# Kernel optimization log

Measured on AMD Instinct MI355X. Metric: run time of the kernel, lower is better.

Reference implementation:

```python
import jax, jax.numpy as jnp
import numpy as np

MIN_DURATION = 0.0
MAX_DURATION = 75.0
MAX_LEN = 80  # hard-coded output length from regulate_length's slice/pad to 80
LN_EPS = 1e-6


def _conv1d_same(x, w, b):
    # x: [B, T, Cin], w: [K, Cin, Cout] -> [B, T, Cout]
    y = jax.lax.conv_general_dilated(
        x, w, window_strides=(1,), padding='SAME',
        dimension_numbers=('NWC', 'WIO', 'NWC'))
    return y + b


def _layernorm(x, gamma, beta):
    mu = jnp.mean(x, axis=-1, keepdims=True)
    var = jnp.mean(jnp.square(x - mu), axis=-1, keepdims=True)
    return (x - mu) * jax.lax.rsqrt(var + LN_EPS) * gamma + beta


def setup_inputs() -> dict:
    key = jax.random.key(0)
    ks = jax.random.split(key, 5)
    B, T, D, F, K = 2048, 128, 256, 256, 3
    scale = 0.05
    return {
        'encoder_output': jax.random.normal(ks[0], (B, T, D), jnp.float32),
        'conv1_w': jax.random.normal(ks[1], (K, D, F), jnp.float32) * scale,
        'conv1_b': jnp.zeros((F,), jnp.float32),
        'conv2_w': jax.random.normal(ks[2], (K, F, F), jnp.float32) * scale,
        'conv2_b': jnp.zeros((F,), jnp.float32),
        'ln_gamma': jnp.ones((F,), jnp.float32),
        'ln_beta': jnp.zeros((F,), jnp.float32),
        'dense_w': jax.random.normal(ks[3], (F, 1), jnp.float32) * scale,
        'dense_b': jnp.full((1,), 2.0, jnp.float32),  # bias so rounded durations are nontrivial
    }


def reference(encoder_output, conv1_w, conv1_b, conv2_w, conv2_b,
              ln_gamma, ln_beta, dense_w, dense_b):
    # --- variance predictor (dropout = identity at inference) ---
    x = jax.nn.relu(_conv1d_same(encoder_output, conv1_w, conv1_b))
    x = _layernorm(x, ln_gamma, ln_beta)
    x = jax.nn.relu(_conv1d_same(x, conv2_w, conv2_b))
    x = _layernorm(x, ln_gamma, ln_beta)
    predicted_durations = x @ dense_w + dense_b  # [B, T, 1]

    # --- regulate_length, fully vectorized over batch ---
    dur = jnp.round(jnp.clip(predicted_durations, MIN_DURATION, MAX_DURATION))
    dur = dur[..., 0].astype(jnp.int32)                 # [B, T]
    cum = jnp.cumsum(dur, axis=1)                       # [B, T]
    pos = jnp.arange(MAX_LEN, dtype=jnp.int32)          # [80]
    # source index for each output frame: searchsorted(cum, pos, side='right')
    idx = jnp.sum(pos[None, :, None] >= cum[:, None, :], axis=-1)  # [B, 80]
    valid = pos[None, :] < cum[:, -1:]                  # [B, 80]
    T = encoder_output.shape[1]
    gathered = jnp.take_along_axis(
        encoder_output, jnp.clip(idx, 0, T - 1)[..., None], axis=1)  # [B, 80, D]
    regulated = jnp.where(valid[..., None], gathered, 0.0)
    return regulated
```

## Files before the change

### kernel.cpp

```cpp
#include <hip/hip_runtime.h>
#include <hip/hip_bf16.h>
#include <math.h>

#define TT 128
#define CC 256
#define MAXLEN 80
#define KSTEPS 24
#define SLOTS 130
#define NCH16 32

typedef __attribute__((ext_vector_type(8))) _Float16 half8v;
typedef __attribute__((ext_vector_type(4))) float f32x4;

#define MSCALE 4096.0f
#define MINV   (1.0f/4096.0f)

__device__ __forceinline__ int chunk(int slot, int c16) {
    return slot * NCH16 + (c16 ^ (slot & 7));
}

__global__ void va_prep(const float* __restrict__ w1, const float* __restrict__ w2,
                        half8v* __restrict__ wsB)
{
    const int idx = blockIdx.x * 256 + threadIdx.x;
    const int lane = idx & 63;
    int q = idx >> 6;
    const int nfg = q & 15;   q >>= 4;
    const int plane = q & 1;  q >>= 1;
    const int kk2 = q & 7;    q >>= 3;
    const int tap = q % 3;
    const int cv  = q / 3;
    const float* w = cv ? w2 : w1;
    const int co  = nfg * 16 + (lane & 15);
    const int ci0 = kk2 * 32 + (lane >> 4) * 8;
    half8v out;
    #pragma unroll
    for (int j = 0; j < 8; ++j) {
        const float x = w[tap * (CC * CC) + (ci0 + j) * CC + co];
        const _Float16 h = (_Float16)x;
        if (plane == 0) out[j] = h;
        else            out[j] = (_Float16)((x - (float)h) * MSCALE);
    }
    wsB[idx] = out;
}

__global__ __launch_bounds__(512, 2)
void va_mfma(const float* __restrict__ enc,
             const float* __restrict__ b1g, const float* __restrict__ b2g,
             const float* __restrict__ gg,  const float* __restrict__ bbg,
             const float* __restrict__ dwg, const float* __restrict__ dbg,
             const half8v* __restrict__ wsB,
             float* __restrict__ outg)
{
    __shared__ half8v P[2][SLOTS * NCH16];
    __shared__ float sumS[8][TT];
    __shared__ float muS[TT];
    __shared__ float rsS[TT];
    __shared__ int   durS[TT];
    __shared__ int   cumS[TT];
    __shared__ int   wtotS[2];

    const int b    = blockIdx.x;
    const int tid  = threadIdx.x;
    const int wid  = tid >> 6;
    const int lane = tid & 63;
    const int l15  = lane & 15;
    const int lg   = lane >> 4;

    const f32x4* encB4 = reinterpret_cast<const f32x4*>(enc) + (size_t)b * (TT * 64);

    for (int m = tid; m < SLOTS * NCH16; m += 512) {
        const int slot = m >> 5;
        const int c16  = m & 31;
        half8v h8, m8;
        if (slot >= 1 && slot <= TT) {
            const f32x4* src = encB4 + (slot - 1) * 64 + c16 * 2;
            const f32x4 v0 = src[0], v1 = src[1];
            #pragma unroll
            for (int j = 0; j < 8; ++j) {
                const float x = (j < 4) ? v0[j] : v1[j - 4];
                const _Float16 h = (_Float16)x;
                h8[j] = h;
                m8[j] = (_Float16)((x - (float)h) * MSCALE);
            }
        } else {
            #pragma unroll
            for (int j = 0; j < 8; ++j) { h8[j] = (_Float16)0.f; m8[j] = (_Float16)0.f; }
        }
        const int ci = chunk(slot, c16);
        P[0][ci] = h8;
        P[1][ci] = m8;
    }
    __syncthreads();

    f32x4 accH[8][2];
    f32x4 accM[8][2];

    float gv[2], bvv[2];
    #pragma unroll
    for (int nf = 0; nf < 2; ++nf) {
        gv[nf]  = gg[wid * 32 + nf * 16 + l15];
        bvv[nf] = bbg[wid * 32 + nf * 16 + l15];
    }

    auto convpass = [&](int cv, const float* __restrict__ biasp, bool first) {
        #pragma unroll
        for (int nf = 0; nf < 2; ++nf) {
            const float bz = biasp[wid * 32 + nf * 16 + l15];
            const f32x4 b4 = {bz, bz, bz, bz};
            const f32x4 z4 = {0.f, 0.f, 0.f, 0.f};
            #pragma unroll
            for (int mf = 0; mf < 8; ++mf) { accH[mf][nf] = b4; accM[mf][nf] = z4; }
        }

        half8v B0[4], B1[4];
        auto loadB = [&](half8v (&Bp)[4], int ks) {
            const int tap = ks >> 3, kk2 = ks & 7;
            #pragma unroll
            for (int p = 0; p < 2; ++p) {
                const int frag = (((cv * 3 + tap) * 8 + kk2) * 2 + p);
                #pragma unroll
                for (int nf = 0; nf < 2; ++nf)
                    Bp[p * 2 + nf] = wsB[(size_t)(frag * 16 + (wid * 2 + nf)) * 64 + lane];
            }
        };
        auto doK = [&](const half8v (&Bp)[4], int ks) {
            const int tap = ks >> 3, kk2 = ks & 7;
            #pragma unroll
            for (int mf = 0; mf < 8; ++mf) {
                const int slot = mf * 16 + l15 + tap;
                const int c16  = kk2 * 4 + lg;
                const int ci = chunk(slot, c16);
                const half8v Ah = P[0][ci];
                const half8v Am = P[1][ci];
                #pragma unroll
                for (int nf = 0; nf < 2; ++nf) {
                    accH[mf][nf] = __builtin_amdgcn_mfma_f32_16x16x32_f16(Ah, Bp[0 * 2 + nf], accH[mf][nf], 0, 0, 0);
                    accM[mf][nf] = __builtin_amdgcn_mfma_f32_16x16x32_f16(Ah, Bp[1 * 2 + nf], accM[mf][nf], 0, 0, 0);
                    accM[mf][nf] = __builtin_amdgcn_mfma_f32_16x16x32_f16(Am, Bp[0 * 2 + nf], accM[mf][nf], 0, 0, 0);
                }
            }
        };

        loadB(B0, 0);
        #pragma unroll 1
        for (int ks = 0; ks < KSTEPS; ks += 2) {
            loadB(B1, ks + 1);
            doK(B0, ks);
            if (ks + 2 < KSTEPS) loadB(B0, ks + 2);
            doK(B1, ks + 1);
        }

        #pragma unroll
        for (int mf = 0; mf < 8; ++mf)
            #pragma unroll
            for (int nf = 0; nf < 2; ++nf) {
                f32x4 v;
                #pragma unroll
                for (int e = 0; e < 4; ++e)
                    v[e] = fmaxf(fmaf(accM[mf][nf][e], MINV, accH[mf][nf][e]), 0.f);
                accH[mf][nf] = v;
            }

        #pragma unroll
        for (int mf = 0; mf < 8; ++mf)
            #pragma unroll
            for (int r = 0; r < 4; ++r) {
                float s = accH[mf][0][r] + accH[mf][1][r];
                s += __shfl_xor(s, 1, 64); s += __shfl_xor(s, 2, 64);
                s += __shfl_xor(s, 4, 64); s += __shfl_xor(s, 8, 64);
                if (l15 == 0) sumS[wid][mf * 16 + lg * 4 + r] = s;
            }
        __syncthreads();
        if (tid < TT) {
            float t = 0.f;
            #pragma unroll
            for (int w = 0; w < 8; ++w) t += sumS[w][tid];
            muS[tid] = t * (1.f / 256.f);
        }
        __syncthreads();
        #pragma unroll
        for (int mf = 0; mf < 8; ++mf)
            #pragma unroll
            for (int r = 0; r < 4; ++r) {
                const float mu = muS[mf * 16 + lg * 4 + r];
                float q = 0.f;
                #pragma unroll
                for (int nf = 0; nf < 2; ++nf) {
                    const float d = accH[mf][nf][r] - mu;
                    q = fmaf(d, d, q);
                }
                q += __shfl_xor(q, 1, 64); q += __shfl_xor(q, 2, 64);
                q += __shfl_xor(q, 4, 64); q += __shfl_xor(q, 8, 64);
                if (l15 == 0) sumS[wid][mf * 16 + lg * 4 + r] = q;
            }
        __syncthreads();
        if (tid < TT) {
            float t = 0.f;
            #pragma unroll
            for (int w = 0; w < 8; ++w) t += sumS[w][tid];
            rsS[tid] = 1.0f / sqrtf(t * (1.f / 256.f) + 1e-6f);
        }
        __syncthreads();
        _Float16* Ph = (_Float16*)&P[0][0];
        _Float16* Pm = (_Float16*)&P[1][0];
        #pragma unroll
        for (int mf = 0; mf < 8; ++mf)
            #pragma unroll
            for (int r = 0; r < 4; ++r) {
                const int row = mf * 16 + lg * 4 + r;
                const float mu = muS[row];
                const float rs = rsS[row];
                #pragma unroll
                for (int nf = 0; nf < 2; ++nf) {
                    const float v = (accH[mf][nf][r] - mu) * rs * gv[nf] + bvv[nf];
                    if (first) {
                        const int col = wid * 32 + nf * 16 + l15;
                        const int slot = row + 1;
                        const int off = chunk(slot, col >> 3) * 8 + (col & 7);
                        const _Float16 h = (_Float16)v;
                        Ph[off] = h;
                        Pm[off] = (_Float16)((v - (float)h) * MSCALE);
                    } else {
                        accH[mf][nf][r] = v;
                    }
                }
            }
    };

    convpass(0, b1g, true);
    __syncthreads();
    convpass(1, b2g, false);

    {
        float dv[2];
        #pragma unroll
        for (int nf = 0; nf < 2; ++nf) dv[nf] = dwg[wid * 32 + nf * 16 + l15];
        #pragma unroll
        for (int mf = 0; mf < 8; ++mf)
            #pragma unroll
            for (int r = 0; r < 4; ++r) {
                float p = accH[mf][0][r] * dv[0] + accH[mf][1][r] * dv[1];
                p += __shfl_xor(p, 1, 64); p += __shfl_xor(p, 2, 64);
                p += __shfl_xor(p, 4, 64); p += __shfl_xor(p, 8, 64);
                if (l15 == 0) sumS[wid][mf * 16 + lg * 4 + r] = p;
            }
        __syncthreads();
        if (tid < TT) {
            float t = 0.f;
            #pragma unroll
            for (int w = 0; w < 8; ++w) t += sumS[w][tid];
            const float pd  = t + dbg[0];
            const float dcl = fminf(fmaxf(pd, 0.0f), 75.0f);
            durS[tid] = (int)rintf(dcl);
        }
        __syncthreads();
    }

    int sv = 0;
    if (tid < TT) {
        sv = durS[tid];
        #pragma unroll
        for (int o = 1; o < 64; o <<= 1) {
            const int u = __shfl_up(sv, o, 64);
            if (lane >= o) sv += u;
        }
        if (lane == 63) wtotS[tid >> 6] = sv;
    }
    __syncthreads();
    if (tid < TT) {
        if (tid >= 64) sv += wtotS[0];
        cumS[tid] = sv;
    }
    __syncthreads();

    const int total = cumS[TT - 1];
    f32x4* outB4 = reinterpret_cast<f32x4*>(outg) + (size_t)b * (MAXLEN * 64);
    for (int pp = 0; pp < 10; ++pp) {
        const int p = wid * 10 + pp;
        int lo = 0, hi = TT;
        while (lo < hi) {
            const int mid = (lo + hi) >> 1;
            if (cumS[mid] <= p) lo = mid + 1; else hi = mid;
        }
        f32x4 v = {0.f, 0.f, 0.f, 0.f};
        if (p < total) {
            const int src = (lo < TT) ? lo : (TT - 1);
            v = encB4[src * 64 + lane];
        }
        outB4[p * 64 + lane] = v;
    }
}

extern "C" void kernel_launch(void* const* d_in, const int* in_sizes, int n_in,
                              void* d_out, int out_size, void* d_ws, size_t ws_size,
                              hipStream_t stream) {
    const float* enc = (const float*)d_in[0];
    const float* w1  = (const float*)d_in[1];
    const float* b1  = (const float*)d_in[2];
    const float* w2  = (const float*)d_in[3];
    const float* b2  = (const float*)d_in[4];
    const float* gam = (const float*)d_in[5];
    const float* bet = (const float*)d_in[6];
    const float* dw  = (const float*)d_in[7];
    const float* db  = (const float*)d_in[8];
    float* out = (float*)d_out;
    half8v* wsB = (half8v*)d_ws;

    const int B = in_sizes[0] / (TT * CC);
    hipLaunchKernelGGL(va_prep, dim3(384), dim3(256), 0, stream, w1, w2, wsB);
    hipLaunchKernelGGL(va_mfma, dim3(B), dim3(512), 0, stream,
                       enc, b1, b2, gam, bet, dw, db, wsB, out);
}
```

Measured before the change: 771.8 us.

## Retile conv MFMA warps to 2x4 grid and fuse layernorm statistics pass

Changes the per-warp tile from all 128 rows by 32 columns to 64 rows by 64 columns (2 row groups by 4 column groups). Each LDS A-fragment read now feeds four N-fragments instead of two, which roughly halves LDS traffic per MFMA. Global weight loads per warp double. Layernorm mean and variance are now computed in one pass as sum and sum of squares, which removes two barriers but risks cancellation error in E[x^2]-mu^2. The fp16 hi/lo split now uses a packed cvt_pkrtz conversion, whose round-toward-zero rounding differs from the old round-to-nearest cast.

```diff
diff --git a/kernel.cpp b/kernel.cpp
--- a/kernel.cpp
+++ b/kernel.cpp
@@ -10,13 +10,20 @@
 #define NCH16 32
 
 typedef __attribute__((ext_vector_type(8))) _Float16 half8v;
+typedef __attribute__((ext_vector_type(2))) _Float16 half2v;
 typedef __attribute__((ext_vector_type(4))) float f32x4;
 
 #define MSCALE 4096.0f
 #define MINV   (1.0f/4096.0f)
 
-__device__ __forceinline__ int chunk(int slot, int c16) {
+__device__ __forceinline__ int chunkidx(int slot, int c16) {
     return slot * NCH16 + (c16 ^ (slot & 7));
+}
+
+__device__ __forceinline__ void split2(float x0, float x1, half2v& h, half2v& m) {
+    h = __builtin_bit_cast(half2v, __builtin_amdgcn_cvt_pkrtz(x0, x1));
+    m.x = (_Float16)fmaf((float)h.x, -MSCALE, x0 * MSCALE);
+    m.y = (_Float16)fmaf((float)h.y, -MSCALE, x1 * MSCALE);
 }
 
 __global__ void va_prep(const float* __restrict__ w1, const float* __restrict__ w2,
@@ -53,7 +60,8 @@
              float* __restrict__ outg)
 {
     __shared__ half8v P[2][SLOTS * NCH16];
-    __shared__ float sumS[8][TT];
+    __shared__ float sumS[4][TT];
+    __shared__ float sumQ[4][TT];
     __shared__ float muS[TT];
     __shared__ float rsS[TT];
     __shared__ int   durS[TT];
@@ -66,78 +74,78 @@
     const int lane = tid & 63;
     const int l15  = lane & 15;
     const int lg   = lane >> 4;
+    const int MGr  = (wid >> 2) * 64;
+    const int NG   = wid & 3;
+    const int NGc  = NG * 64;
 
     const f32x4* encB4 = reinterpret_cast<const f32x4*>(enc) + (size_t)b * (TT * 64);
 
-    for (int m = tid; m < SLOTS * NCH16; m += 512) {
-        const int slot = m >> 5;
-        const int c16  = m & 31;
+    for (int m2 = tid; m2 < SLOTS * NCH16; m2 += 512) {
+        const int slot = m2 >> 5;
+        const int c16  = m2 & 31;
         half8v h8, m8;
         if (slot >= 1 && slot <= TT) {
             const f32x4* src = encB4 + (slot - 1) * 64 + c16 * 2;
             const f32x4 v0 = src[0], v1 = src[1];
-            #pragma unroll
-            for (int j = 0; j < 8; ++j) {
-                const float x = (j < 4) ? v0[j] : v1[j - 4];
-                const _Float16 h = (_Float16)x;
-                h8[j] = h;
-                m8[j] = (_Float16)((x - (float)h) * MSCALE);
-            }
+            half2v hp, mp;
+            split2(v0.x, v0.y, hp, mp); h8[0]=hp.x; h8[1]=hp.y; m8[0]=mp.x; m8[1]=mp.y;
+            split2(v0.z, v0.w, hp, mp); h8[2]=hp.x; h8[3]=hp.y; m8[2]=mp.x; m8[3]=mp.y;
+            split2(v1.x, v1.y, hp, mp); h8[4]=hp.x; h8[5]=hp.y; m8[4]=mp.x; m8[5]=mp.y;
+            split2(v1.z, v1.w, hp, mp); h8[6]=hp.x; h8[7]=hp.y; m8[6]=mp.x; m8[7]=mp.y;
         } else {
             #pragma unroll
             for (int j = 0; j < 8; ++j) { h8[j] = (_Float16)0.f; m8[j] = (_Float16)0.f; }
         }
-        const int ci = chunk(slot, c16);
+        const int ci = chunkidx(slot, c16);
         P[0][ci] = h8;
         P[1][ci] = m8;
     }
     __syncthreads();
 
-    f32x4 accH[8][2];
-    f32x4 accM[8][2];
-
-    float gv[2], bvv[2];
+    f32x4 accH[4][4];
+    f32x4 accM[4][4];
+
+    float gv[4], bvv[4];
     #pragma unroll
-    for (int nf = 0; nf < 2; ++nf) {
-        gv[nf]  = gg[wid * 32 + nf * 16 + l15];
-        bvv[nf] = bbg[wid * 32 + nf * 16 + l15];
+    for (int nf = 0; nf < 4; ++nf) {
+        gv[nf]  = gg[NGc + nf * 16 + l15];
+        bvv[nf] = bbg[NGc + nf * 16 + l15];
     }
 
     auto convpass = [&](int cv, const float* __restrict__ biasp, bool first) {
         #pragma unroll
-        for (int nf = 0; nf < 2; ++nf) {
-            const float bz = biasp[wid * 32 + nf * 16 + l15];
+        for (int nf = 0; nf < 4; ++nf) {
+            const float bz = biasp[NGc + nf * 16 + l15];
             const f32x4 b4 = {bz, bz, bz, bz};
             const f32x4 z4 = {0.f, 0.f, 0.f, 0.f};
             #pragma unroll
-            for (int mf = 0; mf < 8; ++mf) { accH[mf][nf] = b4; accM[mf][nf] = z4; }
-        }
-
-        half8v B0[4], B1[4];
-        auto loadB = [&](half8v (&Bp)[4], int ks) {
+            for (int mf = 0; mf < 4; ++mf) { accH[mf][nf] = b4; accM[mf][nf] = z4; }
+        }
+
+        half8v B0[8], B1[8];
+        auto loadB = [&](half8v (&Bp)[8], int ks) {
             const int tap = ks >> 3, kk2 = ks & 7;
-            #pragma unroll
-            for (int p = 0; p < 2; ++p) {
-                const int frag = (((cv * 3 + tap) * 8 + kk2) * 2 + p);
-                #pragma unroll
-                for (int nf = 0; nf < 2; ++nf)
-                    Bp[p * 2 + nf] = wsB[(size_t)(frag * 16 + (wid * 2 + nf)) * 64 + lane];
-            }
+            const int fb = ((cv * 3 + tap) * 8 + kk2) * 2;
+            #pragma unroll
+            for (int p = 0; p < 2; ++p)
+                #pragma unroll
+                for (int nf = 0; nf < 4; ++nf)
+                    Bp[p * 4 + nf] = wsB[(size_t)((fb + p) * 16 + (NG * 4 + nf)) * 64 + lane];
         };
-        auto doK = [&](const half8v (&Bp)[4], int ks) {
+        auto doK = [&](const half8v (&Bp)[8], int ks) {
             const int tap = ks >> 3, kk2 = ks & 7;
             #pragma unroll
-            for (int mf = 0; mf < 8; ++mf) {
-                const int slot = mf * 16 + l15 + tap;
+            for (int mf = 0; mf < 4; ++mf) {
+                const int slot = MGr + mf * 16 + l15 + tap;
                 const int c16  = kk2 * 4 + lg;
-                const int ci = chunk(slot, c16);
+                const int ci = chunkidx(slot, c16);
                 const half8v Ah = P[0][ci];
                 const half8v Am = P[1][ci];
                 #pragma unroll
-                for (int nf = 0; nf < 2; ++nf) {
-                    accH[mf][nf] = __builtin_amdgcn_mfma_f32_16x16x32_f16(Ah, Bp[0 * 2 + nf], accH[mf][nf], 0, 0, 0);
-                    accM[mf][nf] = __builtin_amdgcn_mfma_f32_16x16x32_f16(Ah, Bp[1 * 2 + nf], accM[mf][nf], 0, 0, 0);
-                    accM[mf][nf] = __builtin_amdgcn_mfma_f32_16x16x32_f16(Am, Bp[0 * 2 + nf], accM[mf][nf], 0, 0, 0);
+                for (int nf = 0; nf < 4; ++nf) {
+                    accH[mf][nf] = __builtin_amdgcn_mfma_f32_16x16x32_f16(Ah, Bp[nf],     accH[mf][nf], 0, 0, 0);
+                    accM[mf][nf] = __builtin_amdgcn_mfma_f32_16x16x32_f16(Ah, Bp[4 + nf], accM[mf][nf], 0, 0, 0);
+                    accM[mf][nf] = __builtin_amdgcn_mfma_f32_16x16x32_f16(Am, Bp[nf],     accM[mf][nf], 0, 0, 0);
                 }
             }
         };
@@ -152,9 +160,9 @@
         }
 
         #pragma unroll
-        for (int mf = 0; mf < 8; ++mf)
-            #pragma unroll
-            for (int nf = 0; nf < 2; ++nf) {
+        for (int mf = 0; mf < 4; ++mf)
+            #pragma unroll
+            for (int nf = 0; nf < 4; ++nf) {
                 f32x4 v;
                 #pragma unroll
                 for (int e = 0; e < 4; ++e)
@@ -163,64 +171,54 @@
             }
 
         #pragma unroll
-        for (int mf = 0; mf < 8; ++mf)
+        for (int mf = 0; mf < 4; ++mf)
             #pragma unroll
             for (int r = 0; r < 4; ++r) {
-                float s = accH[mf][0][r] + accH[mf][1][r];
-                s += __shfl_xor(s, 1, 64); s += __shfl_xor(s, 2, 64);
-                s += __shfl_xor(s, 4, 64); s += __shfl_xor(s, 8, 64);
-                if (l15 == 0) sumS[wid][mf * 16 + lg * 4 + r] = s;
+                float s = (accH[mf][0][r] + accH[mf][1][r]) + (accH[mf][2][r] + accH[mf][3][r]);
+                float q = accH[mf][0][r] * accH[mf][0][r];
+                q = fmaf(accH[mf][1][r], accH[mf][1][r], q);
+                q = fmaf(accH[mf][2][r], accH[mf][2][r], q);
+                q = fmaf(accH[mf][3][r], accH[mf][3][r], q);
+                #pragma unroll
+                for (int o = 1; o < 16; o <<= 1) {
+                    s += __shfl_xor(s, o, 64);
+                    q += __shfl_xor(q, o, 64);
+                }
+                if (l15 == 0) {
+                    const int row = MGr + mf * 16 + lg * 4 + r;
+                    sumS[NG][row] = s;
+                    sumQ[NG][row] = q;
+                }
             }
         __syncthreads();
         if (tid < TT) {
-            float t = 0.f;
-            #pragma unroll
-            for (int w = 0; w < 8; ++w) t += sumS[w][tid];
-            muS[tid] = t * (1.f / 256.f);
-        }
-        __syncthreads();
-        #pragma unroll
-        for (int mf = 0; mf < 8; ++mf)
-            #pragma unroll
-            for (int r = 0; r < 4; ++r) {
-                const float mu = muS[mf * 16 + lg * 4 + r];
-                float q = 0.f;
-                #pragma unroll
-                for (int nf = 0; nf < 2; ++nf) {
-                    const float d = accH[mf][nf][r] - mu;
-                    q = fmaf(d, d, q);
-                }
-                q += __shfl_xor(q, 1, 64); q += __shfl_xor(q, 2, 64);
-                q += __shfl_xor(q, 4, 64); q += __shfl_xor(q, 8, 64);
-                if (l15 == 0) sumS[wid][mf * 16 + lg * 4 + r] = q;
-            }
-        __syncthreads();
-        if (tid < TT) {
-            float t = 0.f;
-            #pragma unroll
-            for (int w = 0; w < 8; ++w) t += sumS[w][tid];
-            rsS[tid] = 1.0f / sqrtf(t * (1.f / 256.f) + 1e-6f);
+            const float S = (sumS[0][tid] + sumS[1][tid]) + (sumS[2][tid] + sumS[3][tid]);
+            const float Q = (sumQ[0][tid] + sumQ[1][tid]) + (sumQ[2][tid] + sumQ[3][tid]);
+            const float mu = S * (1.f / 256.f);
+            const float var = fmaf(-mu, mu, Q * (1.f / 256.f));
+            muS[tid] = mu;
+            rsS[tid] = 1.0f / sqrtf(var + 1e-6f);
         }
         __syncthreads();
         _Float16* Ph = (_Float16*)&P[0][0];
         _Float16* Pm = (_Float16*)&P[1][0];
         #pragma unroll
-        for (int mf = 0; mf < 8; ++mf)
+        for (int mf = 0; mf < 4; ++mf)
             #pragma unroll
             for (int r = 0; r < 4; ++r) {
-                const int row = mf * 16 + lg * 4 + r;
+                const int row = MGr + mf * 16 + lg * 4 + r;
                 const float mu = muS[row];
                 const float rs = rsS[row];
                 #pragma unroll
-                for (int nf = 0; nf < 2; ++nf) {
+                for (int nf = 0; nf < 4; ++nf) {
                     const float v = (accH[mf][nf][r] - mu) * rs * gv[nf] + bvv[nf];
                     if (first) {
-                        const int col = wid * 32 + nf * 16 + l15;
+                        const int col = NGc + nf * 16 + l15;
                         const int slot = row + 1;
-                        const int off = chunk(slot, col >> 3) * 8 + (col & 7);
+                        const int off = chunkidx(slot, col >> 3) * 8 + (col & 7);
                         const _Float16 h = (_Float16)v;
                         Ph[off] = h;
-                        Pm[off] = (_Float16)((v - (float)h) * MSCALE);
+                        Pm[off] = (_Float16)fmaf((float)h, -MSCALE, v * MSCALE);
                     } else {
                         accH[mf][nf][r] = v;
                     }
@@ -233,24 +231,22 @@
     convpass(1, b2g, false);
 
     {
-        float dv[2];
-        #pragma unroll
-        for (int nf = 0; nf < 2; ++nf) dv[nf] = dwg[wid * 32 + nf * 16 + l15];
-        #pragma unroll
-        for (int mf = 0; mf < 8; ++mf)
+        float dv[4];
+        #pragma unroll
+        for (int nf = 0; nf < 4; ++nf) dv[nf] = dwg[NGc + nf * 16 + l15];
+        #pragma unroll
+        for (int mf = 0; mf < 4; ++mf)
             #pragma unroll
             for (int r = 0; r < 4; ++r) {
-                float p = accH[mf][0][r] * dv[0] + accH[mf][1][r] * dv[1];
-                p += __shfl_xor(p, 1, 64); p += __shfl_xor(p, 2, 64);
-                p += __shfl_xor(p, 4, 64); p += __shfl_xor(p, 8, 64);
-                if (l15 == 0) sumS[wid][mf * 16 + lg * 4 + r] = p;
+                float p = (accH[mf][0][r] * dv[0] + accH[mf][1][r] * dv[1])
+                        + (accH[mf][2][r] * dv[2] + accH[mf][3][r] * dv[3]);
+                #pragma unroll
+                for (int o = 1; o < 16; o <<= 1) p += __shfl_xor(p, o, 64);
+                if (l15 == 0) sumS[NG][MGr + mf * 16 + lg * 4 + r] = p;
             }
         __syncthreads();
         if (tid < TT) {
-            float t = 0.f;
-            #pragma unroll
-            for (int w = 0; w < 8; ++w) t += sumS[w][tid];
-            const float pd  = t + dbg[0];
+            const float pd = (sumS[0][tid] + sumS[1][tid]) + (sumS[2][tid] + sumS[3][tid]) + dbg[0];
             const float dcl = fminf(fmaxf(pd, 0.0f), 75.0f);
             durS[tid] = (int)rintf(dcl);
         }
```

Result: faster. 654.7 us (-15.2%).
